# Kernel optimization log

Measured on AMD Instinct MI355X. Metric: run time of the kernel, lower is better.

The kernel has to match this reference:

```python
import jax, jax.numpy as jnp
import numpy as np

K = 3  # spline order
G = 5  # grid_size

def bspline(x):
    # Cox-de Boor B-spline basis over uniform grid on [-1,1] extended by K knots each side.
    h = 2.0 / G
    grid = jnp.arange(-K, G + K + 1, dtype=x.dtype) * h - 1.0  # [G+2K+1]
    xe = x[..., None]
    b = ((xe >= grid[:-1]) & (xe < grid[1:])).astype(x.dtype)  # order-0 bases [..., G+2K]
    for p in range(1, K + 1):
        b = ((xe - grid[:-(p + 1)]) / (grid[p:-1] - grid[:-(p + 1)]) * b[..., :-1]
             + (grid[p + 1:] - xe) / (grid[p + 1:] - grid[1:-p]) * b[..., 1:])
    return b  # [..., G+K]

def kan_conv(x, wb, ws, k):
    # x: [B,Cin,H,W] -> patches [B, Cin*k*k, H', W'] -> KANLinear per spatial position
    p = jax.lax.conv_general_dilated_patches(x, (k, k), (1, 1), 'VALID')
    p = jnp.moveaxis(p, 1, -1)  # [B,H',W',F]
    base = jax.nn.silu(p) @ wb.T
    spline = jnp.einsum('bhwig,oig->bhwo', bspline(p), ws)
    return jnp.moveaxis(base + spline, -1, 1)  # [B,Cout,H',W']

def maxpool2(x):
    return jax.lax.reduce_window(x, -jnp.inf, jax.lax.max, (1, 1, 2, 2), (1, 1, 2, 2), 'VALID')

def setup_inputs() -> dict:
    key = jax.random.key(0)
    ks = jax.random.split(key, 9)
    B = 4096
    s = 0.1
    return {
        'x': jax.random.normal(ks[0], (B, 1, 28, 28), jnp.float32),
        'wb1': jax.random.normal(ks[1], (5, 9), jnp.float32) * s,
        'ws1': jax.random.normal(ks[2], (5, 9, G + K), jnp.float32) * s,
        'wb2': jax.random.normal(ks[3], (5, 125), jnp.float32) * s,
        'ws2': jax.random.normal(ks[4], (5, 125, G + K), jnp.float32) * s,
        'wb3': jax.random.normal(ks[5], (2, 45), jnp.float32) * s,
        'ws3': jax.random.normal(ks[6], (2, 45, G + K), jnp.float32) * s,
        'fc_w': jax.random.normal(ks[7], (200, 98), jnp.float32) * s,
        'fc_b': jnp.zeros((200,), jnp.float32),
    }

def reference(x, wb1, ws1, wb2, ws2, wb3, ws3, fc_w, fc_b):
    h = kan_conv(x, wb1, ws1, 3)    # [B,5,26,26]
    h = maxpool2(h)                 # [B,5,13,13]
    h = kan_conv(h, wb2, ws2, 5)    # [B,5,9,9]
    h = kan_conv(h, wb3, ws3, 3)    # [B,2,7,7]
    h = h.reshape(h.shape[0], -1)   # [B,98]
    return h @ fc_w.T + fc_b        # [B,200]
```

## Files before the change

kernel.cpp:

```cpp
#include <hip/hip_runtime.h>


typedef _Float16 h2 __attribute__((ext_vector_type(2)));
typedef _Float16 f16x8 __attribute__((ext_vector_type(8)));
typedef float f32x4 __attribute__((ext_vector_type(4)));
typedef unsigned int uint_t;
typedef unsigned long long u64;

__device__ __forceinline__ h2 as_h2(uint_t u) { union { uint_t u; h2 h; } c; c.u = u; return c.h; }
__device__ __forceinline__ uint_t pk(float a, float b) {
    h2 v; v[0] = (_Float16)a; v[1] = (_Float16)b;
    union { h2 h; uint_t u; } c; c.h = v; return c.u;
}

__device__ __forceinline__ float fdot2f(h2 a, h2 b, float c) {
#if __has_builtin(__builtin_amdgcn_fdot2)
    return __builtin_amdgcn_fdot2(a, b, c, false);
#else
    return c + (float)a[0] * (float)b[0] + (float)a[1] * (float)b[1];
#endif
}

__device__ __forceinline__ float silu_f(float v) {
    return v / (1.0f + __expf(-v));
}

__device__ __forceinline__ void write_rec16(_Float16* p, float v) {
    float s  = silu_f(v);
    float t  = (v + 2.2f) * 2.5f;
    float cf = floorf(t);
    int   c  = (int)cf;
    float u  = t - cf;
    float u2 = u * u, u3 = u2 * u;
    float w  = 1.0f - u;
    const float k6 = 0.16666667f;
    float n0 = k6 * u3;
    float n1 = k6 * (-3.0f * u3 + 3.0f * u2 + 3.0f * u + 1.0f);
    float n2 = k6 * (3.0f * u3 - 6.0f * u2 + 4.0f);
    float n3 = k6 * (w * w * w);
    u64 H = ((u64)pk(n1, n0) << 32) | (u64)pk(n3, n2);
    if ((unsigned)c > 10u) H = 0;
    int cc = c < 0 ? 0 : (c > 10 ? 10 : c);
    int L  = cc * 16 - 48;
    u64 sl_lo = (L < 64) ? (H << (L & 63)) : 0;
    u64 hi_a  = (L == 0) ? 0 : (H >> ((64 - L) & 63));
    u64 hi_b  = H << ((L - 64) & 63);
    u64 sl_hi = (L < 64) ? hi_a : hi_b;
    u64 sr    = H >> ((-L) & 63);
    u64 B0 = (L >= 0) ? sl_lo : sr;
    u64 B1 = (L >= 0) ? sl_hi : 0;
    u64    R0 = (B0 << 16) | (u64)pk(s, 0.0f);
    u64    R1 = (B0 >> 48) | (B1 << 16);
    uint_t R2 = (uint_t)(B1 >> 48);
    uint4 lo, hi;
    lo.x = (uint_t)R0; lo.y = (uint_t)(R0 >> 32);
    lo.z = (uint_t)R1; lo.w = (uint_t)(R1 >> 32);
    hi.x = R2; hi.y = 0; hi.z = 0; hi.w = 0;
    *(uint4*)(p)     = lo;
    *(uint4*)(p + 8) = hi;
}

struct Rec { h2 a[5]; };
__device__ __forceinline__ Rec load_rec16(const _Float16* p) {
    uint4  u0 = *(const uint4*)(p);
    uint_t u2 = *(const uint_t*)(p + 8);
    Rec r;
    r.a[0] = as_h2(u0.x); r.a[1] = as_h2(u0.y);
    r.a[2] = as_h2(u0.z); r.a[3] = as_h2(u0.w);
    r.a[4] = as_h2(u2);
    return r;
}

#define W3_OFF 6700
#define FCWT_BYTE_OFF  15360
#define W1COL_BYTE_OFF 93760
#define W2COL_BYTE_OFF 95680

__global__ __launch_bounds__(256) void kan_prep(
    const float* __restrict__ wb1, const float* __restrict__ ws1,
    const float* __restrict__ wb2, const float* __restrict__ ws2,
    const float* __restrict__ wb3, const float* __restrict__ ws3,
    const float* __restrict__ fcw, _Float16* __restrict__ w16,
    float* __restrict__ fcwT)
{
    _Float16* w1col = (_Float16*)((char*)w16 + W1COL_BYTE_OFF);
    _Float16* w2col = (_Float16*)((char*)w16 + W2COL_BYTE_OFF);
    int gtid = blockIdx.x * 256 + threadIdx.x;
    int gstr = gridDim.x * 256;
    for (int i = gtid; i < 760; i += gstr) {
        const float *wb, *ws; int r;
        if (i < 45)       { wb = wb1; ws = ws1; r = i; }
        else if (i < 670) { wb = wb2; ws = ws2; r = i - 45; }
        else              { wb = wb3; ws = ws3; r = i - 670; }
        _Float16* p = w16 + i * 10;
        p[0] = (_Float16)wb[r];
#pragma unroll
        for (int g = 0; g < 8; ++g) p[1 + g] = (_Float16)ws[r * 8 + g];
        p[9] = (_Float16)0.0f;
    }
    for (int i = gtid; i < 19600; i += gstr) {
        int o = i / 98, j = i % 98;
        fcwT[j * 200 + o] = fcw[i];
    }
    for (int i = gtid; i < 960; i += gstr) {
        int n = i / 160, k = i % 160;
        int rec = k >> 4, f = k & 15;
        float v = 0.f;
        if (n < 5 && rec < 9 && f < 10)
            v = (f == 0) ? wb1[n * 9 + rec] : ws1[(n * 9 + rec) * 8 + (f - 1)];
        w1col[i] = (_Float16)v;
    }
    for (int i = gtid; i < 14400; i += gstr) {
        int n = i / 2400, k = i % 2400;
        int R = k >> 4, f = k & 15;
        int c = R / 30, rem = R % 30, di = rem / 6, dj = rem % 6;
        float v = 0.f;
        if (n < 5 && dj < 5 && f < 10) {
            int r = n * 125 + c * 25 + di * 5 + dj;
            v = (f == 0) ? wb2[r] : ws2[r * 8 + (f - 1)];
        }
        w2col[i] = (_Float16)v;
    }
}

__global__ __launch_bounds__(256) void kan_fused(
    const float* __restrict__ x,
    const _Float16* __restrict__ w16,
    const _Float16* __restrict__ w1col,
    const _Float16* __restrict__ w2col,
    const float* __restrict__ fcwT,
    const float* __restrict__ fcb,
    float* __restrict__ out)
{
    __shared__ __align__(16) _Float16 smemA[13600];
    __shared__ __align__(16) float    smemB[2048];
    _Float16* P2h   = (_Float16*)smemB;
    float*    part2 = smemB;
    float*    part3 = smemB;
    float*    h3f   = smemB + 1024;

    const int b   = blockIdx.x;
    const int tid = threadIdx.x;
    const int wv  = __builtin_amdgcn_readfirstlane(tid >> 6);
    const int ln  = tid & 63;

    const int m   = ln & 15;
    const int kb  = ln >> 4;
    const int hr  = kb >> 1;
    const int s8  = (kb & 1) * 8;
    const int nn  = m < 5 ? m : 5;

#pragma unroll 1
    for (int i = tid; i < 784; i += 256)
        write_rec16(&smemA[i * 16], x[b * 784 + i]);
    __syncthreads();

    {
        f16x8 Bf[5];
#pragma unroll
        for (int ks = 0; ks < 5; ++ks)
            Bf[ks] = *(const f16x8*)(w1col + nn * 160 + ks * 32 + kb * 8);
        const int offT[10] = {0, 16, 32, 448, 464, 480, 896, 912, 928, 0};
#pragma unroll 1
        for (int tile = wv; tile < 43; tile += 4) {
            int p = tile * 16 + m; p = p > 675 ? 675 : p;
            int y = p / 26, xx = p % 26;
            int basep = (y * 28 + xx) * 16 + s8;
            f32x4 acc = {0.f, 0.f, 0.f, 0.f};
#pragma unroll
            for (int ks = 0; ks < 5; ++ks) {
                int sel = hr ? offT[2 * ks + 1] : offT[2 * ks];
                f16x8 av = *(const f16x8*)(smemA + basep + sel);
                acc = __builtin_amdgcn_mfma_f32_16x16x32_f16(av, Bf[ks], acc, 0, 0, 0);
            }
            int srow = tile * 16 + (ln >> 4) * 4;
#pragma unroll
            for (int r = 0; r < 4; ++r) {
                int s = srow + r;
                if (m < 5 && s < 676) P2h[m * 676 + s] = (_Float16)acc[r];
            }
        }
    }
    __syncthreads();

#pragma unroll 1
    for (int i = tid; i < 845; i += 256) {
        int c = i / 169, pp = i % 169;
        int ph = pp / 13, pw = pp % 13;
        const _Float16* q = P2h + c * 676 + (2 * ph) * 26 + 2 * pw;
        h2 a = as_h2(*(const uint_t*)q);
        h2 d = as_h2(*(const uint_t*)(q + 26));
        float mx = fmaxf(fmaxf((float)a[0], (float)a[1]),
                         fmaxf((float)d[0], (float)d[1]));
        write_rec16(&smemA[pp * 80 + c * 16], mx);
    }
    if (tid < 10) {
        uint4 z; z.x = 0; z.y = 0; z.z = 0; z.w = 0;
        *(uint4*)(&smemA[13520 + tid * 8]) = z;
    }
    __syncthreads();

    {
        int ryb[6];
#pragma unroll
        for (int t = 0; t < 6; ++t) {
            int p = t * 16 + m; p = p > 80 ? 80 : p;
            ryb[t] = (p / 9) * 13 + (p % 9);
        }
        f32x4 acc[6];
#pragma unroll
        for (int t = 0; t < 6; ++t) { f32x4 z = {0.f,0.f,0.f,0.f}; acc[t] = z; }
#pragma unroll 1
        for (int pr = wv; pr < 25; pr += 4) {
            int c = pr / 5, di = pr % 5;
            const _Float16* wrow = w2col + nn * 2400 + pr * 96 + kb * 8;
            int cbase = c * 16 + s8;
            int rb = di * 13;
#pragma unroll
            for (int ks = 0; ks < 3; ++ks) {
                f16x8 bv = *(const f16x8*)(wrow + ks * 32);
                int rp_off = rb + 2 * ks + hr;
#pragma unroll
                for (int t = 0; t < 6; ++t) {
                    int rp = ryb[t] + rp_off;
                    f16x8 av = *(const f16x8*)(smemA + rp * 80 + cbase);
                    acc[t] = __builtin_amdgcn_mfma_f32_16x16x32_f16(av, bv, acc[t], 0, 0, 0);
                }
            }
        }
        int prow = (ln >> 4) * 4;
#pragma unroll
        for (int t = 0; t < 6; ++t) {
#pragma unroll
            for (int r = 0; r < 4; ++r) {
                int pp = t * 16 + prow + r;
                if (m < 5 && pp < 81) part2[(wv * 5 + m) * 81 + pp] = acc[t][r];
            }
        }
    }
    __syncthreads();

#pragma unroll 1
    for (int i = tid; i < 405; i += 256) {
        int o = i / 81, pp = i % 81;
        float v = part2[(0 * 5 + o) * 81 + pp] + part2[(1 * 5 + o) * 81 + pp]
                + part2[(2 * 5 + o) * 81 + pp] + part2[(3 * 5 + o) * 81 + pp];
        write_rec16(&smemA[pp * 80 + o * 16], v);
    }
    __syncthreads();

#pragma unroll 1
    for (int c = wv; c < 5; c += 4) {
        if (ln < 49) {
            int pp = ln;
            int y = pp / 7, xx = pp % 7;
            float acc[2] = {0.f, 0.f};
#pragma unroll 1
            for (int di = 0; di < 3; ++di) {
                const _Float16* base = &smemA[((y + di) * 9 + xx) * 80 + c * 16];
                Rec r[3];
#pragma unroll
                for (int p = 0; p < 3; ++p) r[p] = load_rec16(base + p * 80);
#pragma unroll
                for (int o = 0; o < 2; ++o) {
                    const h2* w = (const h2*)(w16 + (W3_OFF + (o * 45 + c * 9 + di * 3) * 10));
                    float a = acc[o];
#pragma unroll
                    for (int dj = 0; dj < 3; ++dj)
#pragma unroll
                        for (int q = 0; q < 5; ++q)
                            a = fdot2f(r[dj].a[q], w[dj * 5 + q], a);
                    acc[o] = a;
                }
            }
            part3[(c * 2 + 0) * 49 + pp] = acc[0];
            part3[(c * 2 + 1) * 49 + pp] = acc[1];
        }
    }
    __syncthreads();

    if (tid < 98) {
        int o = tid / 49, pp = tid % 49;
        float v = part3[(0 * 2 + o) * 49 + pp] + part3[(1 * 2 + o) * 49 + pp]
                + part3[(2 * 2 + o) * 49 + pp] + part3[(3 * 2 + o) * 49 + pp]
                + part3[(4 * 2 + o) * 49 + pp];
        h3f[tid] = v;
    }
    __syncthreads();

    if (tid < 200) {
        float a0 = 0.f, a1 = 0.f;
#pragma unroll 7
        for (int j = 0; j < 98; j += 2) {
            a0 += fcwT[j * 200 + tid]       * h3f[j];
            a1 += fcwT[(j + 1) * 200 + tid] * h3f[j + 1];
        }
        out[b * 200 + tid] = fcb[tid] + a0 + a1;
    }
}

extern "C" void kernel_launch(void* const* d_in, const int* in_sizes, int n_in,
                              void* d_out, int out_size, void* d_ws, size_t ws_size,
                              hipStream_t stream) {
    const float* x   = (const float*)d_in[0];
    const float* wb1 = (const float*)d_in[1];
    const float* ws1 = (const float*)d_in[2];
    const float* wb2 = (const float*)d_in[3];
    const float* ws2 = (const float*)d_in[4];
    const float* wb3 = (const float*)d_in[5];
    const float* ws3 = (const float*)d_in[6];
    const float* fcw = (const float*)d_in[7];
    const float* fcb = (const float*)d_in[8];
    float* out = (float*)d_out;

    _Float16* w16   = (_Float16*)d_ws;
    float*    fcwT  = (float*)((char*)d_ws + FCWT_BYTE_OFF);
    _Float16* w1col = (_Float16*)((char*)d_ws + W1COL_BYTE_OFF);
    _Float16* w2col = (_Float16*)((char*)d_ws + W2COL_BYTE_OFF);

    kan_prep<<<32, 256, 0, stream>>>(wb1, ws1, wb2, ws2, wb3, ws3, fcw, w16, fcwT);

    int B = in_sizes[0] / 784;
    kan_fused<<<B, 256, 0, stream>>>(x, w16, w1col, w2col, fcwT, fcb, out);
}
```

Measured before the change: 156.3 us.

## Repack conv2 patches per tap and swizzle conv1 records in LDS

The stage-1 input records are written with an XOR swizzle of their two 8-half chunks, which is meant to cut LDS bank conflicts on the conv1 MFMA A-operand loads. The pooled stage-2 records are packed densely at 10 halves per channel (72 halves per pixel) instead of 16, and the conv2 weight matrix is rebuilt to match. Conv2 now loops over the 25 kernel taps, doing 2 MFMAs per tap instead of 3 per channel-row. The aim is fewer MFMA steps, less zero-padding work and less LDS, traded for unaligned packed records and tighter buffer sizing in shared memory.

```diff
diff --git a/kernel.cpp b/kernel.cpp
--- a/kernel.cpp
+++ b/kernel.cpp
@@ -25,7 +25,8 @@
     return v / (1.0f + __expf(-v));
 }
 
-__device__ __forceinline__ void write_rec16(_Float16* p, float v) {
+struct RecW { u64 R0, R1; uint_t R2; };
+__device__ __forceinline__ RecW rec_words(float v) {
     float s  = silu_f(v);
     float t  = (v + 2.2f) * 2.5f;
     float cf = floorf(t);
@@ -49,15 +50,29 @@
     u64 sr    = H >> ((-L) & 63);
     u64 B0 = (L >= 0) ? sl_lo : sr;
     u64 B1 = (L >= 0) ? sl_hi : 0;
-    u64    R0 = (B0 << 16) | (u64)pk(s, 0.0f);
-    u64    R1 = (B0 >> 48) | (B1 << 16);
-    uint_t R2 = (uint_t)(B1 >> 48);
+    RecW r;
+    r.R0 = (B0 << 16) | (u64)pk(s, 0.0f);
+    r.R1 = (B0 >> 48) | (B1 << 16);
+    r.R2 = (uint_t)(B1 >> 48);
+    return r;
+}
+
+__device__ __forceinline__ void write_rec16s(_Float16* p, int off, float v) {
+    RecW rw = rec_words(v);
     uint4 lo, hi;
-    lo.x = (uint_t)R0; lo.y = (uint_t)(R0 >> 32);
-    lo.z = (uint_t)R1; lo.w = (uint_t)(R1 >> 32);
-    hi.x = R2; hi.y = 0; hi.z = 0; hi.w = 0;
-    *(uint4*)(p)     = lo;
-    *(uint4*)(p + 8) = hi;
+    lo.x = (uint_t)rw.R0; lo.y = (uint_t)(rw.R0 >> 32);
+    lo.z = (uint_t)rw.R1; lo.w = (uint_t)(rw.R1 >> 32);
+    hi.x = rw.R2; hi.y = 0; hi.z = 0; hi.w = 0;
+    *(uint4*)(p + off)       = lo;
+    *(uint4*)(p + (8 ^ off)) = hi;
+}
+
+__device__ __forceinline__ void write_rec10(_Float16* p, float v) {
+    RecW rw = rec_words(v);
+    uint_t* d = (uint_t*)p;
+    d[0] = (uint_t)rw.R0; d[1] = (uint_t)(rw.R0 >> 32);
+    d[2] = (uint_t)rw.R1; d[3] = (uint_t)(rw.R1 >> 32);
+    d[4] = rw.R2;
 }
 
 struct Rec { h2 a[5]; };
@@ -110,12 +125,13 @@
             v = (f == 0) ? wb1[n * 9 + rec] : ws1[(n * 9 + rec) * 8 + (f - 1)];
         w1col[i] = (_Float16)v;
     }
-    for (int i = gtid; i < 14400; i += gstr) {
-        int n = i / 2400, k = i % 2400;
-        int R = k >> 4, f = k & 15;
-        int c = R / 30, rem = R % 30, di = rem / 6, dj = rem % 6;
+    for (int i = gtid; i < 9600; i += gstr) {
+        int n = i / 1600, k2 = i % 1600;
+        int tap = k2 >> 6, k = k2 & 63;
+        int di = tap / 5, dj = tap % 5;
+        int c = k / 10, f = k % 10;
         float v = 0.f;
-        if (n < 5 && dj < 5 && f < 10) {
+        if (n < 5 && k < 50 && f < 9) {
             int r = n * 125 + c * 25 + di * 5 + dj;
             v = (f == 0) ? wb2[r] : ws2[r * 8 + (f - 1)];
         }
@@ -132,12 +148,12 @@
     const float* __restrict__ fcb,
     float* __restrict__ out)
 {
-    __shared__ __align__(16) _Float16 smemA[13600];
-    __shared__ __align__(16) float    smemB[2048];
+    __shared__ __align__(16) _Float16 smemA[12544];
+    __shared__ __align__(16) float    smemB[1696];
     _Float16* P2h   = (_Float16*)smemB;
     float*    part2 = smemB;
     float*    part3 = smemB;
-    float*    h3f   = smemB + 1024;
+    float*    h3f   = smemB + 512;
 
     const int b   = blockIdx.x;
     const int tid = threadIdx.x;
@@ -152,7 +168,7 @@
 
 #pragma unroll 1
     for (int i = tid; i < 784; i += 256)
-        write_rec16(&smemA[i * 16], x[b * 784 + i]);
+        write_rec16s(&smemA[i * 16], (i & 4) << 1, x[b * 784 + i]);
     __syncthreads();
 
     {
@@ -160,17 +176,18 @@
 #pragma unroll
         for (int ks = 0; ks < 5; ++ks)
             Bf[ks] = *(const f16x8*)(w1col + nn * 160 + ks * 32 + kb * 8);
-        const int offT[10] = {0, 16, 32, 448, 464, 480, 896, 912, 928, 0};
+        const int dpix[10] = {0, 1, 2, 28, 29, 30, 56, 57, 58, 0};
 #pragma unroll 1
         for (int tile = wv; tile < 43; tile += 4) {
             int p = tile * 16 + m; p = p > 675 ? 675 : p;
-            int y = p / 26, xx = p % 26;
-            int basep = (y * 28 + xx) * 16 + s8;
+            int pix0 = (p / 26) * 28 + (p % 26);
             f32x4 acc = {0.f, 0.f, 0.f, 0.f};
 #pragma unroll
             for (int ks = 0; ks < 5; ++ks) {
-                int sel = hr ? offT[2 * ks + 1] : offT[2 * ks];
-                f16x8 av = *(const f16x8*)(smemA + basep + sel);
+                int dp = hr ? dpix[2 * ks + 1] : dpix[2 * ks];
+                int p2 = pix0 + dp;
+                int addr = p2 * 16 + (s8 ^ ((p2 & 4) << 1));
+                f16x8 av = *(const f16x8*)(smemA + addr);
                 acc = __builtin_amdgcn_mfma_f32_16x16x32_f16(av, Bf[ks], acc, 0, 0, 0);
             }
             int srow = tile * 16 + (ln >> 4) * 4;
@@ -192,11 +209,7 @@
         h2 d = as_h2(*(const uint_t*)(q + 26));
         float mx = fmaxf(fmaxf((float)a[0], (float)a[1]),
                          fmaxf((float)d[0], (float)d[1]));
-        write_rec16(&smemA[pp * 80 + c * 16], mx);
-    }
-    if (tid < 10) {
-        uint4 z; z.x = 0; z.y = 0; z.z = 0; z.w = 0;
-        *(uint4*)(&smemA[13520 + tid * 8]) = z;
+        write_rec10(&smemA[pp * 72 + c * 10], mx);
     }
     __syncthreads();
 
@@ -211,21 +224,19 @@
 #pragma unroll
         for (int t = 0; t < 6; ++t) { f32x4 z = {0.f,0.f,0.f,0.f}; acc[t] = z; }
 #pragma unroll 1
-        for (int pr = wv; pr < 25; pr += 4) {
-            int c = pr / 5, di = pr % 5;
-            const _Float16* wrow = w2col + nn * 2400 + pr * 96 + kb * 8;
-            int cbase = c * 16 + s8;
-            int rb = di * 13;
-#pragma unroll
-            for (int ks = 0; ks < 3; ++ks) {
-                f16x8 bv = *(const f16x8*)(wrow + ks * 32);
-                int rp_off = rb + 2 * ks + hr;
-#pragma unroll
-                for (int t = 0; t < 6; ++t) {
-                    int rp = ryb[t] + rp_off;
-                    f16x8 av = *(const f16x8*)(smemA + rp * 80 + cbase);
-                    acc[t] = __builtin_amdgcn_mfma_f32_16x16x32_f16(av, bv, acc[t], 0, 0, 0);
-                }
+        for (int tap = wv; tap < 25; tap += 4) {
+            int di = tap / 5, dj = tap % 5;
+            const _Float16* wrow = w2col + nn * 1600 + tap * 64 + kb * 8;
+            f16x8 bv0 = *(const f16x8*)(wrow);
+            f16x8 bv1 = *(const f16x8*)(wrow + 32);
+            int qoff = di * 13 + dj;
+#pragma unroll
+            for (int t = 0; t < 6; ++t) {
+                const _Float16* ab = smemA + (ryb[t] + qoff) * 72 + kb * 8;
+                acc[t] = __builtin_amdgcn_mfma_f32_16x16x32_f16(
+                             *(const f16x8*)(ab), bv0, acc[t], 0, 0, 0);
+                acc[t] = __builtin_amdgcn_mfma_f32_16x16x32_f16(
+                             *(const f16x8*)(ab + 32), bv1, acc[t], 0, 0, 0);
             }
         }
         int prow = (ln >> 4) * 4;
@@ -245,7 +256,7 @@
         int o = i / 81, pp = i % 81;
         float v = part2[(0 * 5 + o) * 81 + pp] + part2[(1 * 5 + o) * 81 + pp]
                 + part2[(2 * 5 + o) * 81 + pp] + part2[(3 * 5 + o) * 81 + pp];
-        write_rec16(&smemA[pp * 80 + o * 16], v);
+        write_rec16s(&smemA[pp * 80 + o * 16], 0, v);
     }
     __syncthreads();
 
```

New measurement: 148.4 us. 1.05x faster.
